# Performance work log

Measured on AMD Instinct MI355X. Metric: run time of the kernel, lower is better.

The kernel has to match this reference:

```python
import jax, jax.numpy as jnp
import numpy as np

B, N, K = 4, 1024, 512
HEADS, DH = 8, 64
HID = 2048
KAPPA = 1.0      # kappa_beta
ALPHA = 1e-3     # ffn_alpha (prior weight)
LAM = 1.0        # ffn_lambda_belief
NITER = 2        # ffn_n_iterations
EPS = 1e-8


def _ln(x, g, b):
    m = jnp.mean(x, axis=-1, keepdims=True)
    v = jnp.var(x, axis=-1, keepdims=True)
    return (x - m) * jax.lax.rsqrt(v + 1e-5) * g + b


def _transport(x, phi, G):
    # truncated exp(phi . G) applied to x without materializing (B,N,K,K)
    def Ax(y):
        return jnp.einsum('bng,gkl,bnl->bnk', phi, G, y)
    a1 = Ax(x)
    return x + a1 + 0.5 * Ax(a1)


def setup_inputs() -> dict:
    key = jax.random.key(0)
    ks = jax.random.split(key, 16)
    mu_q = jax.random.normal(ks[0], (B, N, K), dtype=jnp.float32)
    sigma_q = jax.random.uniform(ks[1], (B, N, K), minval=0.5, maxval=1.5, dtype=jnp.float32)
    phi = 0.1 * jax.random.normal(ks[2], (B, N, 3), dtype=jnp.float32)
    A = jax.random.normal(ks[3], (3, K, K), dtype=jnp.float32)
    generators = 0.05 * (A - jnp.transpose(A, (0, 2, 1)))  # antisymmetric Lie generators
    mask = jnp.broadcast_to(jnp.tril(jnp.ones((N, N), dtype=bool)), (B, N, N))  # causal
    mu_prior = jax.random.normal(ks[4], (B, N, K), dtype=jnp.float32)
    s = 0.02
    Wq = s * jax.random.normal(ks[5], (K, K), dtype=jnp.float32)
    Wk = s * jax.random.normal(ks[6], (K, K), dtype=jnp.float32)
    Wv = s * jax.random.normal(ks[7], (K, K), dtype=jnp.float32)
    Wo = s * jax.random.normal(ks[8], (K, K), dtype=jnp.float32)
    g1 = jnp.ones((K,), jnp.float32); be1 = jnp.zeros((K,), jnp.float32)
    g2 = jnp.ones((K,), jnp.float32); be2 = jnp.zeros((K,), jnp.float32)
    W1 = s * jax.random.normal(ks[9], (K, HID), dtype=jnp.float32)
    bh1 = jnp.zeros((HID,), jnp.float32)
    W2 = s * jax.random.normal(ks[10], (HID, K), dtype=jnp.float32)
    bh2 = jnp.zeros((K,), jnp.float32)
    lr = jnp.array(0.1, jnp.float32)  # learnable VFE step size
    return {'mu_q': mu_q, 'sigma_q': sigma_q, 'phi': phi, 'generators': generators,
            'mask': mask, 'mu_prior': mu_prior, 'Wq': Wq, 'Wk': Wk, 'Wv': Wv, 'Wo': Wo,
            'g1': g1, 'be1': be1, 'g2': g2, 'be2': be2,
            'W1': W1, 'bh1': bh1, 'W2': W2, 'bh2': bh2, 'lr': lr}


def reference(mu_q, sigma_q, phi, generators, mask, mu_prior,
              Wq, Wk, Wv, Wo, g1, be1, g2, be2, W1, bh1, W2, bh2, lr):
    # ---- attention sublayer ----
    mu_n = _ln(mu_q, g1, be1)
    mu_g = _transport(mu_n, phi, generators)  # transport to common frame

    def heads(x):  # (B,N,K) -> (B,H,N,Dh)
        return x.reshape(B, N, HEADS, DH).transpose(0, 2, 1, 3)

    q = heads(mu_g @ Wq)
    k = heads(mu_g @ Wk)
    v = heads(mu_g @ Wv)
    # diagonal covariance propagated through linear maps: var_out = sigma @ W^2
    sq = heads(sigma_q @ (Wq * Wq)) + EPS
    sk = heads(sigma_q @ (Wk * Wk)) + EPS

    inv = 1.0 / sq
    # KL(N(k_j,sk_j) || N(q_i,sq_i)) for diagonal Gaussians, decomposed into matmuls
    tr = jnp.einsum('bhid,bhjd->bhij', inv, sk)
    quad = (jnp.sum(q * q * inv, axis=-1)[..., None]
            - 2.0 * jnp.einsum('bhid,bhjd->bhij', q * inv, k)
            + jnp.einsum('bhid,bhjd->bhij', inv, k * k))
    logdet = (jnp.sum(jnp.log(sq), axis=-1)[..., None]
              - jnp.sum(jnp.log(sk), axis=-1)[:, :, None, :])
    kl = 0.5 * (tr + quad - DH + logdet)  # (B,H,N,N)

    scores = jnp.where(mask[:, None, :, :], -kl / KAPPA, -1e9)
    beta = jax.nn.softmax(scores, axis=-1)

    out = jnp.einsum('bhij,bhjd->bhid', beta, v)
    out = out.transpose(0, 2, 1, 3).reshape(B, N, K)
    mu_attn = _transport(out @ Wo, -phi, generators)  # back-transport to local frames
    mu_res = mu_q + mu_attn  # residual (dropout is identity in eval)

    # ---- VFE_dynamic FFN sublayer ----
    mu_n2 = _ln(mu_res, g2, be2)
    beta_m = jnp.mean(beta, axis=1)  # (B,N,N) attention-belief coupling
    h = mu_n2
    for _ in range(NITER):
        drive = jax.nn.gelu(h @ W1 + bh1) @ W2 + bh2
        grad = ALPHA * (h - mu_prior) + LAM * (h - jnp.einsum('bij,bjk->bik', beta_m, h))
        h = h + lr * (drive - grad)
    mu_out = mu_res + (h - mu_n2)

    return (mu_out, sigma_q, phi)
```

## Files before the change

### kernel.cpp

```cpp
#include <hip/hip_runtime.h>
#include <math.h>

#define BB 4
#define NN 1024
#define KK 512
#define HH 8
#define DHh 64
#define HIDd 2048
#define BN (BB*NN)

typedef unsigned short u16;
typedef __attribute__((ext_vector_type(8))) short bf16x8;
typedef __attribute__((ext_vector_type(4))) float f32x4;

__device__ __forceinline__ float gelu_tanh(float x){
    float x3 = x*x*x;
    float t = tanhf(0.7978845608028654f*(x + 0.044715f*x3));
    return 0.5f*x*(1.0f+t);
}
__device__ __forceinline__ u16 f2bf(float x){
    unsigned int u = __float_as_uint(x);
    unsigned int r = (u + 0x7fffu + ((u>>16)&1u)) >> 16;
    return (u16)r;
}
__device__ __forceinline__ float bf2f(u16 b){
    return __uint_as_float(((unsigned int)b)<<16);
}
__device__ __forceinline__ void gload16(const void* g, void* l){
    __builtin_amdgcn_global_load_lds((__attribute__((address_space(1))) void*)g,
                                     (__attribute__((address_space(3))) void*)l, 16, 0, 0);
}
__device__ __forceinline__ void wsplit(u16* hi, u16* lo, size_t o, float v){
    u16 h = f2bf(v);
    hi[o] = h;
    if (lo) lo[o] = f2bf(v - bf2f(h));
}

__global__ __launch_bounds__(256) void split_t_k(
    const float* __restrict__ src, u16* __restrict__ hi, u16* __restrict__ lo,
    int Kc, int Nc, long sS, long sD, int square)
{
    __shared__ float t[32][33];
    const int n0 = blockIdx.x*32, k0 = blockIdx.y*32, bz = blockIdx.z;
    const float* S = src + (long)bz*sS;
    const int tx = threadIdx.x & 31, ty = threadIdx.x >> 5;
    for (int r = ty; r < 32; r += 8){
        float v = S[(long)(k0+r)*Nc + n0+tx];
        if (square) v *= v;
        t[r][tx] = v;
    }
    __syncthreads();
    for (int r = ty; r < 32; r += 8){
        float v = t[tx][r];
        long o = (long)bz*sD + (long)(n0+r)*Kc + k0 + tx;
        wsplit(hi, lo, o, v);
    }
}

__global__ __launch_bounds__(256) void wmega_k(
    const float* __restrict__ Wq, const float* __restrict__ Wk,
    const float* __restrict__ Wv, const float* __restrict__ Wo,
    const float* __restrict__ W1, const float* __restrict__ W2,
    const float* __restrict__ gen,
    u16* __restrict__ WQKVh, u16* __restrict__ WQKVl, u16* __restrict__ WoTh,
    u16* __restrict__ WSQKh, u16* __restrict__ WSQKl,
    u16* __restrict__ W1Th, u16* __restrict__ W2Th, u16* __restrict__ GFh)
{
    const int z = blockIdx.z;
    const int tid = threadIdx.x;
    if (z == 8){
        if (blockIdx.x >= 48) return;
        const int c0 = blockIdx.x*32, k0 = blockIdx.y*32;
        const int tx = tid&31, ty = tid>>5;
        const int g = c0/KK, l0 = c0%KK;
        for (int r=ty; r<32; r+=8)
            GFh[(size_t)(k0+r)*(3*KK) + c0+tx] =
                f2bf(gen[(size_t)g*KK*KK + (size_t)(k0+r)*KK + l0+tx]);
        return;
    }
    __shared__ float t[32][33];
    const float* src; u16* hi; u16* lo=0; int sq=0;
    int n0, k0, Kc, Nc;
    const size_t KK2 = (size_t)KK*KK;
    if (z < 6){
        if (blockIdx.x >= 16) return;
        n0 = blockIdx.x*32; k0 = blockIdx.y*32; Kc=KK; Nc=KK;
        if      (z==0){ src=Wq; hi=WQKVh;       lo=WQKVl; }
        else if (z==1){ src=Wk; hi=WQKVh+KK2;   lo=WQKVl+KK2; }
        else if (z==2){ src=Wv; hi=WQKVh+2*KK2; lo=WQKVl+2*KK2; }
        else if (z==3){ src=Wo; hi=WoTh; }
        else if (z==4){ src=Wq; hi=WSQKh;       lo=WSQKl; sq=1; }
        else          { src=Wk; hi=WSQKh+KK2;   lo=WSQKl+KK2; sq=1; }
    } else if (z == 6){
        src=W1; hi=W1Th; Kc=KK; Nc=HIDd;
        n0 = blockIdx.x*32; k0 = blockIdx.y*32;
    } else {
        src=W2; hi=W2Th; Kc=HIDd; Nc=KK;
        n0 = blockIdx.y*32; k0 = blockIdx.x*32;
    }
    const int tx=tid&31, ty=tid>>5;
    for (int r=ty;r<32;r+=8){
        float v = src[(long)(k0+r)*Nc + n0+tx];
        if (sq) v*=v;
        t[r][tx]=v;
    }
    __syncthreads();
    for (int r=ty;r<32;r+=8){
        float v = t[tx][r];
        long o = (long)(n0+r)*Kc + k0+tx;
        wsplit(hi, lo, o, v);
    }
}

template<int PRODS>
__global__ __launch_bounds__(256) void gemm_mfma_k(
    const u16* __restrict__ Ah, const u16* __restrict__ Al,
    const u16* __restrict__ Bh, const u16* __restrict__ Bl,
    float* __restrict__ C, u16* __restrict__ Chi, u16* __restrict__ Clo,
    int M, int Kc, int Nc, int lda,
    long sA, long sB, long sC, const float* __restrict__ bias, int act,
    int cskip)
{
    __shared__ u16 shAh[2][128*32], shBh[2][128*32];
    constexpr int SLO = (PRODS==3) ? 2*128*32 : 8;
    __shared__ u16 shAl[SLO], shBl[SLO];
    const int m0 = blockIdx.x*128, n0 = blockIdx.y*128;
    if (cskip == 1 && n0 > m0 + 127) return;
    const int bz = blockIdx.z;
    const u16* gAh = Ah + (long)bz*sA;
    const u16* gBh = Bh + (long)bz*sB;
    const u16* gAl = (PRODS==3) ? Al + (long)bz*sA : nullptr;
    const u16* gBl = (PRODS==3) ? Bl + (long)bz*sB : nullptr;
    const int tid = threadIdx.x;
    const int wave = tid >> 6, lane = tid & 63;
    const int quad = lane >> 4, r16 = lane & 15;
    const int wm = (wave>>1)*64, wn = (wave&1)*64;

    f32x4 acc[4][4];
    #pragma unroll
    for (int i=0;i<4;i++)
        #pragma unroll
        for (int j=0;j<4;j++) acc[i][j] = (f32x4){0.f,0.f,0.f,0.f};

    auto stage = [&](int sel, int k0){
        #pragma unroll
        for (int half=0; half<2; ++half){
            int c = half*256 + tid;
            int row = c >> 2;
            int kg = ((c & 3) ^ ((row >> 1) & 3))*8;
            long ga = (long)(m0+row)*lda + k0 + kg;
            long gb = (long)(n0+row)*Kc + k0 + kg;
            gload16(gAh+ga, &shAh[sel][c*8]);
            gload16(gBh+gb, &shBh[sel][c*8]);
            if constexpr (PRODS==3){
                gload16(gAl+ga, &shAl[sel*128*32 + c*8]);
                gload16(gBl+gb, &shBl[sel*128*32 + c*8]);
            }
        }
    };

    const int nsteps = Kc >> 5;
    stage(0, 0);
    __syncthreads();
    int cur = 0;
    const int swz = (quad ^ ((r16 >> 1) & 3))*8;
    for (int t = 0; t < nsteps; ++t){
        if (t+1 < nsteps) stage(cur^1, (t+1)<<5);
        bf16x8 afh[4], bfh[4];
        #pragma unroll
        for (int i=0;i<4;i++){
            afh[i] = *(const bf16x8*)&shAh[cur][(wm+i*16+r16)*32 + swz];
            bfh[i] = *(const bf16x8*)&shBh[cur][(wn+i*16+r16)*32 + swz];
        }
        if constexpr (PRODS==3){
            bf16x8 afl[4], bfl[4];
            #pragma unroll
            for (int i=0;i<4;i++){
                afl[i] = *(const bf16x8*)&shAl[cur*128*32 + (wm+i*16+r16)*32 + swz];
                bfl[i] = *(const bf16x8*)&shBl[cur*128*32 + (wn+i*16+r16)*32 + swz];
            }
            #pragma unroll
            for (int i=0;i<4;i++)
                #pragma unroll
                for (int j=0;j<4;j++){
                    acc[i][j] = __builtin_amdgcn_mfma_f32_16x16x32_bf16(afh[i], bfh[j], acc[i][j], 0,0,0);
                    acc[i][j] = __builtin_amdgcn_mfma_f32_16x16x32_bf16(afh[i], bfl[j], acc[i][j], 0,0,0);
                    acc[i][j] = __builtin_amdgcn_mfma_f32_16x16x32_bf16(afl[i], bfh[j], acc[i][j], 0,0,0);
                }
        } else {
            #pragma unroll
            for (int i=0;i<4;i++)
                #pragma unroll
                for (int j=0;j<4;j++)
                    acc[i][j] = __builtin_amdgcn_mfma_f32_16x16x32_bf16(afh[i], bfh[j], acc[i][j], 0,0,0);
        }
        __syncthreads();
        cur ^= 1;
    }
    #pragma unroll
    for (int i=0;i<4;i++){
        #pragma unroll
        for (int j=0;j<4;j++){
            int gc = n0 + wn + j*16 + r16;
            if (gc >= Nc) continue;
            float bv = bias ? bias[gc] : 0.f;
            #pragma unroll
            for (int r=0;r<4;r++){
                long gr = m0 + wm + i*16 + quad*4 + r;
                float v = acc[i][j][r] + bv;
                if (act) v = gelu_tanh(v);
                long o = (long)bz*sC + gr*Nc + gc;
                if (C) C[o] = v;
                if (Chi){ u16 t = f2bf(v); Chi[o] = t; if (Clo) Clo[o] = f2bf(v - bf2f(t)); }
            }
        }
    }
}

__global__ __launch_bounds__(256) void gemm64_k(
    const u16* __restrict__ Ah, const u16* __restrict__ Bh,
    float* __restrict__ C, u16* __restrict__ Chi, u16* __restrict__ Clo,
    int M, int Kc, int Nc, int lda,
    long sA, long sB, long sC, const float* __restrict__ bias, int act,
    int ktrim,
    const float* __restrict__ phi, u16* __restrict__ X3e, float esign,
    const float* __restrict__ t_x, const float* __restrict__ t_a1,
    const float* __restrict__ t_res,
    const float* __restrict__ f_hin, const float* __restrict__ f_bmh,
    const float* __restrict__ f_mup, const float* __restrict__ f_lr,
    u16* __restrict__ f_hh, float* __restrict__ f_hout,
    const float* __restrict__ f_mrb, const float* __restrict__ f_mn2,
    float* __restrict__ f_out, int fmode)
{
    __shared__ u16 shA[2][64*64], shB[2][64*64];
    const int m0 = blockIdx.x*64, n0 = blockIdx.y*64;
    const int bz = blockIdx.z;
    const u16* gA = Ah + (long)bz*sA;
    const u16* gB = Bh + (long)bz*sB;
    const int tid = threadIdx.x;
    const int wave = tid >> 6, lane = tid & 63;
    const int quad = lane >> 4, r16 = lane & 15;
    const int wr = wave*16;
    const int kend = ktrim ? min(Kc, m0 + 64) : Kc;
    const int nsteps = kend >> 6;

    f32x4 acc[4];
    #pragma unroll
    for (int j=0;j<4;j++) acc[j] = (f32x4){0.f,0.f,0.f,0.f};

    auto stage = [&](int sel, int k0){
        #pragma unroll
        for (int rep=0; rep<2; ++rep){
            int c = rep*256 + tid;
            int row = c >> 3;
            int kg = ((c & 7) ^ (row & 7))*8;
            gload16(gA + (long)(m0+row)*lda + k0 + kg, &shA[sel][c*8]);
            gload16(gB + (long)(n0+row)*Kc + k0 + kg, &shB[sel][c*8]);
        }
    };

    stage(0, 0);
    __syncthreads();
    int cur = 0;
    for (int t = 0; t < nsteps; ++t){
        if (t+1 < nsteps) stage(cur^1, (t+1)<<6);
        #pragma unroll
        for (int kk=0; kk<2; ++kk){
            const int s = (((kk<<2)+quad) ^ (r16 & 7))*8;
            bf16x8 af = *(const bf16x8*)&shA[cur][(wr+r16)*64 + s];
            #pragma unroll
            for (int j=0;j<4;j++){
                bf16x8 bh = *(const bf16x8*)&shB[cur][(j*16+r16)*64 + s];
                acc[j] = __builtin_amdgcn_mfma_f32_16x16x32_bf16(af, bh, acc[j], 0,0,0);
            }
        }
        __syncthreads();
        cur ^= 1;
    }
    float lrv = 0.f;
    if (fmode) lrv = *f_lr;
    #pragma unroll
    for (int j=0;j<4;j++){
        int gc = n0 + j*16 + r16;
        float bv = bias ? bias[gc] : 0.f;
        #pragma unroll
        for (int r=0;r<4;r++){
            long gr = m0 + wr + quad*4 + r;
            float v = acc[j][r] + bv;
            if (act) v = gelu_tanh(v);
            long o = (long)bz*sC + gr*Nc + gc;
            if (t_x){
                v = t_x[o] + t_a1[o] + 0.5f*v;
                if (t_res) v += t_res[o];
            }
            if (fmode){
                float hv = f_hin[o];
                float val = hv + lrv*(v - (1e-3f*(hv - f_mup[o]) + (hv - f_bmh[o])));
                if (fmode == 1){ f_hout[o] = val; f_hh[o] = f2bf(val); }
                else           { f_out[o] = f_mrb[o] + val - f_mn2[o]; }
            } else {
                if (C) C[o] = v;
                if (Chi){ u16 t = f2bf(v); Chi[o] = t; if (Clo) Clo[o] = f2bf(v - bf2f(t)); }
                if (X3e){
                    const float* ph = phi + gr*3;
                    size_t b = (size_t)gr*(3*KK) + gc;
                    X3e[b]      = f2bf(esign*ph[0]*v);
                    X3e[b+KK]   = f2bf(esign*ph[1]*v);
                    X3e[b+2*KK] = f2bf(esign*ph[2]*v);
                }
            }
        }
    }
}

__global__ __launch_bounds__(256) void ln_k(
    const float* __restrict__ x, const float* __restrict__ g,
    const float* __restrict__ be, float* __restrict__ y,
    const float* __restrict__ phi, u16* __restrict__ x3, float esign,
    const float* __restrict__ sg, u16* __restrict__ sgh, u16* __restrict__ sgl,
    u16* __restrict__ yh16, float* __restrict__ osig, float* __restrict__ ophi)
{
    __shared__ float sh[8];
    const int r = blockIdx.x, tid = threadIdx.x;
    const float* xr = x + (long)r*KK;
    float2 v = *(const float2*)(xr + tid*2);
    float s = v.x+v.y, s2 = v.x*v.x+v.y*v.y;
    #pragma unroll
    for (int o=32;o>0;o>>=1){ s += __shfl_down(s,o); s2 += __shfl_down(s2,o); }
    if ((tid&63)==0){ sh[tid>>6]=s; sh[4+(tid>>6)]=s2; }
    __syncthreads();
    s  = sh[0]+sh[1]+sh[2]+sh[3];
    s2 = sh[4]+sh[5]+sh[6]+sh[7];
    const float mean = s*(1.f/KK);
    const float var  = s2*(1.f/KK) - mean*mean;
    const float rs = rsqrtf(var + 1e-5f);
    float2 gg = *(const float2*)(g + tid*2);
    float2 bb = *(const float2*)(be + tid*2);
    float ox = (v.x-mean)*rs*gg.x + bb.x;
    float oy = (v.y-mean)*rs*gg.y + bb.y;
    long o = (long)r*KK + tid*2;
    *(float2*)(y + o) = make_float2(ox, oy);
    if (yh16){ yh16[o] = f2bf(ox); yh16[o+1] = f2bf(oy); }
    if (x3){
        const float* ph = phi + r*3;
        size_t b = (size_t)r*(3*KK) + tid*2;
        #pragma unroll
        for (int gg2=0; gg2<3; ++gg2){
            float p = esign*ph[gg2];
            x3[b + gg2*KK]     = f2bf(p*ox);
            x3[b + gg2*KK + 1] = f2bf(p*oy);
        }
        if (ophi && tid < 3) ophi[(size_t)r*3 + tid] = phi[(size_t)r*3 + tid];
    }
    if (sgh){
        float2 sv = *(const float2*)(sg + o);
        wsplit(sgh, sgl, o,   sv.x);
        wsplit(sgh, sgl, o+1, sv.y);
        if (osig) *(float2*)(osig + o) = sv;
    }
}

__global__ __launch_bounds__(512) void prepvt_k(
    const float* __restrict__ QKV, const float* __restrict__ SQSK,
    u16* __restrict__ CFh, u16* __restrict__ CFl,
    u16* __restrict__ KSh, u16* __restrict__ KSl, float* __restrict__ dvec,
    u16* __restrict__ VTh)
{
    __shared__ float t[64][65];
    const int bx = blockIdx.x;
    const int tid = threadIdx.x;
    if (bx < BN){
        const int bn = bx;
        const int b = bn / NN, n = bn % NN;
        const int h = tid >> 6, d = tid & 63;
        float q  = QKV[(size_t)bn*1536 + h*DHh + d];
        float k  = QKV[(size_t)bn*1536 + KK + h*DHh + d];
        float sq = SQSK[(size_t)bn*1024 + h*DHh + d] + 1e-8f;
        float sk = SQSK[(size_t)bn*1024 + KK + h*DHh + d] + 1e-8f;
        float inv = 1.f/sq;
        float nqi = -2.f*q*inv;
        float skk = sk + k*k;
        const size_t base = ((size_t)(h*BB + b)*NN + n)*128;
        wsplit(CFh, CFl, base+d,    inv);
        wsplit(CFh, CFl, base+64+d, nqi);
        wsplit(KSh, KSl, base+d,    skk);
        wsplit(KSh, KSl, base+64+d, k);
        float dv = __logf(sk);
        #pragma unroll
        for (int o=32;o>0;o>>=1) dv += __shfl_down(dv,o);
        if (d==0) dvec[((size_t)h*BB + b)*NN + n] = dv;
        return;
    }
    const int idx = bx - BN;
    const int n0 = (idx & 15)*64;
    const int h = (idx>>4)&7;
    const int b = idx>>7;
    const int c4 = (tid & 15) * 4;
    const int r0 = tid >> 4;
    for (int rr = r0; rr < 64; rr += 32){
        float4 v = *(const float4*)(QKV + (size_t)(b*NN + n0 + rr)*1536 + 1024 + h*DHh + c4);
        t[c4+0][rr] = v.x; t[c4+1][rr] = v.y; t[c4+2][rr] = v.z; t[c4+3][rr] = v.w;
    }
    __syncthreads();
    for (int dd = r0; dd < 64; dd += 32){
        size_t base = ((size_t)(h*BB + b)*64 + dd)*NN + n0 + c4;
        #pragma unroll
        for (int q=0;q<4;q++) VTh[base+q] = f2bf(t[dd][c4+q]);
    }
}

__global__ __launch_bounds__(256) void softmax_all_k(
    float* __restrict__ S, const float* __restrict__ dvec, u16* __restrict__ BMh)
{
    __shared__ float s_sc[NN];
    __shared__ float s_bm[NN];
    __shared__ float s_red[4];
    const int tid = threadIdx.x;
    const int b = blockIdx.x / NN, i = blockIdx.x % NN;
    const int L = i + 1;
    const int JEND = ((i >> 6) + 1) << 6;
    for (int j=tid;j<JEND;j+=256) s_bm[j]=0.f;
    for (int h=0; h<8; ++h){
        const int z = h*BB + b;
        float* row = S + ((long)z*NN + i)*NN;
        const float* dp = dvec + (size_t)z*NN;
        float lm = -3.0e38f;
        for (int j=tid;j<L;j+=256){
            float sc = -0.5f*row[j] + 0.5f*dp[j];
            s_sc[j] = sc;
            lm = fmaxf(lm, sc);
        }
        #pragma unroll
        for (int o=32;o>0;o>>=1) lm = fmaxf(lm, __shfl_xor(lm, o));
        __syncthreads();
        if ((tid&63)==0) s_red[tid>>6] = lm;
        __syncthreads();
        const float mx = fmaxf(fmaxf(s_red[0],s_red[1]), fmaxf(s_red[2],s_red[3]));
        float ps = 0.f;
        for (int j=tid;j<L;j+=256){
            float e = __expf(s_sc[j]-mx);
            s_sc[j] = e;
            ps += e;
        }
        #pragma unroll
        for (int o=32;o>0;o>>=1) ps += __shfl_xor(ps, o);
        __syncthreads();
        if ((tid&63)==0) s_red[tid>>6] = ps;
        __syncthreads();
        const float isum = 1.f/(s_red[0]+s_red[1]+s_red[2]+s_red[3]);
        u16* brow = (u16*)row;
        for (int j=tid;j<JEND;j+=256){
            if (j < L){
                float w = s_sc[j]*isum;
                brow[j] = f2bf(w);
                s_bm[j] += 0.125f*w;
            } else {
                brow[j] = 0;
            }
        }
        __syncthreads();
    }
    const long bmrow = ((long)b*NN + i)*NN;
    for (int j=tid;j<JEND;j+=256) BMh[bmrow+j] = f2bf(s_bm[j]);
}

__global__ __launch_bounds__(256) void pv_k(
    const u16* __restrict__ Sbeta,
    const u16* __restrict__ VTh,
    u16* __restrict__ xh)
{
    __shared__ u16 shA[2][64*64], shB[2][64*64];
    const int m0 = blockIdx.x*64;
    const int z = blockIdx.y;
    const int b = z & 3, head = z >> 2;
    const int tid = threadIdx.x;
    const int wave = tid>>6, lane = tid&63;
    const int quad = lane>>4, r16 = lane&15;
    f32x4 acc[4];
    #pragma unroll
    for (int j=0;j<4;j++) acc[j]=(f32x4){0.f,0.f,0.f,0.f};
    const int nsteps = (m0 >> 6) + 1;

    auto stage = [&](int sel, int j0){
        #pragma unroll
        for (int rep=0; rep<2; ++rep){
            int c = rep*256 + tid;
            int row = c >> 3;
            int k8 = ((c & 7) ^ (row & 7))*8;
            gload16(Sbeta + ((size_t)(z*NN + m0 + row))*(2*NN) + j0 + k8, &shA[sel][c*8]);
            gload16(VTh + ((size_t)(z*64 + row))*NN + j0 + k8, &shB[sel][c*8]);
        }
    };

    stage(0, 0);
    __syncthreads();
    int cur = 0;
    for (int t = 0; t < nsteps; ++t){
        if (t+1 < nsteps) stage(cur^1, (t+1)<<6);
        #pragma unroll
        for (int kk=0; kk<2; ++kk){
            const int s = (((kk<<2)+quad) ^ (r16 & 7))*8;
            bf16x8 af = *(const bf16x8*)&shA[cur][(wave*16 + r16)*64 + s];
            #pragma unroll
            for (int nj=0; nj<4; ++nj){
                bf16x8 bh = *(const bf16x8*)&shB[cur][(nj*16 + r16)*64 + s];
                acc[nj] = __builtin_amdgcn_mfma_f32_16x16x32_bf16(af, bh, acc[nj], 0,0,0);
            }
        }
        __syncthreads();
        cur ^= 1;
    }
    #pragma unroll
    for (int nj=0;nj<4;nj++){
        #pragma unroll
        for (int r=0;r<4;r++){
            int i = m0 + wave*16 + quad*4 + r;
            int d = nj*16 + r16;
            size_t o = ((size_t)(b*NN)+i)*KK + head*64 + d;
            xh[o] = f2bf(acc[nj][r]);
        }
    }
}

extern "C" void kernel_launch(void* const* d_in, const int* in_sizes, int n_in,
                              void* d_out, int out_size, void* d_ws, size_t ws_size,
                              hipStream_t stream) {
    const float* mu_q    = (const float*)d_in[0];
    const float* sigma_q = (const float*)d_in[1];
    const float* phi     = (const float*)d_in[2];
    const float* gen     = (const float*)d_in[3];
    const float* mu_prior= (const float*)d_in[5];
    const float* Wq = (const float*)d_in[6];
    const float* Wk = (const float*)d_in[7];
    const float* Wv = (const float*)d_in[8];
    const float* Wo = (const float*)d_in[9];
    const float* g1 = (const float*)d_in[10];
    const float* be1= (const float*)d_in[11];
    const float* g2 = (const float*)d_in[12];
    const float* be2= (const float*)d_in[13];
    const float* W1 = (const float*)d_in[14];
    const float* bh1= (const float*)d_in[15];
    const float* W2 = (const float*)d_in[16];
    const float* bh2= (const float*)d_in[17];
    const float* lr = (const float*)d_in[18];
    float* out = (float*)d_out;

    float* w = (float*)d_ws;
    size_t off = 0;
    auto alloc = [&](size_t n){ float* p = w + off; off += (n+3)&~(size_t)3; return p; };
    auto ualloc = [&](size_t n){ return (u16*)alloc((n+1)/2); };

    float* Xb   = alloc((size_t)BN*KK);
    float* A1b  = alloc((size_t)BN*KK);
    float* A2b  = alloc((size_t)BN*KK);
    float* QKVb = alloc((size_t)BN*3*KK);
    float* SQSKb= alloc((size_t)BN*2*KK);
    float* REG  = alloc((size_t)16*NN*NN);
    float* Sbig = Xb;
    u16*  X3a   = (u16*)REG;
    u16*  X3b   = X3a + (size_t)BN*3*KK;
    u16*  SGh   = X3b + (size_t)BN*3*KK;
    u16*  SGl   = SGh + (size_t)BN*KK;
    u16*  ZH    = (u16*)REG;
    float* Db_  = alloc((size_t)HH*BB*NN);
    u16* AH  = ualloc((size_t)BN*HIDd); u16* AL  = ualloc((size_t)BN*HIDd);
    u16* CFh = AH;
    u16* CFl = AH + (size_t)HH*BB*NN*128;
    u16* KSh = AL;
    u16* KSl = AL + (size_t)HH*BB*NN*128;
    u16* VTh = ualloc((size_t)HH*BB*64*NN);
    u16* GFh = ualloc((size_t)3*KK*KK);
    u16* WQKVh= ualloc((size_t)3*KK*KK); u16* WQKVl= ualloc((size_t)3*KK*KK);
    u16* WSQKh= ualloc((size_t)2*KK*KK); u16* WSQKl= ualloc((size_t)2*KK*KK);
    u16* WoTh= ualloc((size_t)KK*KK);
    u16* W1Th= ualloc((size_t)KK*HIDd);
    u16* W2Th= ualloc((size_t)KK*HIDd);
    u16* BMh = ualloc((size_t)BB*NN*NN);
    u16* HTh = ualloc((size_t)BB*KK*NN);
    float* WOb = QKVb;
    float* Hb  = QKVb + (size_t)BN*KK;
    float* MRb = QKVb + 2*(size_t)BN*KK;
    float* MN2b= Xb;
    (void)A2b; (void)SQSKb;

    auto gemm64 = [&](const u16* ah, const u16* bh,
                      float* C, u16* chi, u16* clo, int M, int Kc, int Nc, int lda,
                      long sA, long sB, long sC, const float* bias, int act,
                      int ktrim, const float* xphi, u16* x3e, float esign,
                      const float* tx, const float* ta1, const float* tres, int batch){
        dim3 g(M/64, Nc/64, batch);
        gemm64_k<<<g, 256, 0, stream>>>(ah, bh, C, chi, clo,
                                        M, Kc, Nc, lda, sA, sB, sC, bias, act, ktrim,
                                        xphi, x3e, esign, tx, ta1, tres,
                                        0,0,0,0,0,0,0,0,0,0);
    };

    {
        dim3 gw(64, 16, 9);
        wmega_k<<<gw, 256, 0, stream>>>(Wq, Wk, Wv, Wo, W1, W2, gen,
                                        WQKVh, WQKVl, WoTh, WSQKh, WSQKl,
                                        W1Th, W2Th, GFh);
    }

    ln_k<<<BN, 256, 0, stream>>>(mu_q, g1, be1, Xb, phi, X3a, 1.f, sigma_q, SGh, SGl,
                                 0, out + (size_t)BN*KK, out + 2*(size_t)BN*KK);
    gemm64(X3a, GFh, A1b, 0,0, BN, 3*KK, KK, 3*KK, 0,0,0, nullptr, 0, 0,
           phi, X3b, 1.f, 0,0,0, 1);
    gemm64(X3b, GFh, 0, AH, AL, BN, 3*KK, KK, 3*KK, 0,0,0, nullptr, 0, 0,
           0, 0, 0.f, Xb, A1b, 0, 1);

    {
        dim3 gq(BN/128, (3*KK)/128, 1);
        gemm_mfma_k<3><<<gq, 256, 0, stream>>>(AH, AL, WQKVh, WQKVl, QKVb, 0, 0,
            BN, KK, 3*KK, KK, 0, 0, 0, nullptr, 0, 0);
        dim3 gs(BN/128, (2*KK)/128, 1);
        gemm_mfma_k<3><<<gs, 256, 0, stream>>>(SGh, SGl, WSQKh, WSQKl, SQSKb, 0, 0,
            BN, KK, 2*KK, KK, 0, 0, 0, nullptr, 0, 0);
    }
    prepvt_k<<<BN + 512, 512, 0, stream>>>(QKVb, SQSKb, CFh, CFl, KSh, KSl, Db_, VTh);

    {
        dim3 sg(NN/128, NN/128, 32);
        gemm_mfma_k<3><<<sg, 256, 0, stream>>>(CFh, CFl, KSh, KSl,
            Sbig, 0, 0, NN, 128, NN, 128,
            (long)NN*128, (long)NN*128, (long)NN*NN, nullptr, 0, 1);
        softmax_all_k<<<BB*NN, 256, 0, stream>>>(Sbig, Db_, BMh);
        dim3 pg(NN/64, 32, 1);
        pv_k<<<pg, 256, 0, stream>>>((const u16*)Sbig, VTh, AH);
    }

    gemm64(AH, WoTh, WOb, 0,0, BN, KK, KK, KK, 0,0,0, nullptr, 0, 0,
           phi, X3a, -1.f, 0,0,0, 1);
    gemm64(X3a, GFh, A1b, 0,0, BN, 3*KK, KK, 3*KK, 0,0,0, nullptr, 0, 0,
           phi, X3b, -1.f, 0,0,0, 1);
    gemm64(X3b, GFh, MRb, 0,0, BN, 3*KK, KK, 3*KK, 0,0,0, nullptr, 0, 0,
           0, 0, 0.f, WOb, A1b, mu_q, 1);
    ln_k<<<BN, 256, 0, stream>>>(MRb, g2, be2, MN2b, 0, 0, 0.f, 0, 0, 0,
                                 AH, 0, 0);

    for (int it=0; it<2; ++it){
        const float* hin = (it==0) ? MN2b : Hb;
        {
            dim3 tg(KK/32, NN/32, BB);
            split_t_k<<<tg, 256, 0, stream>>>(hin, HTh, 0, NN, KK,
                                              (long)NN*KK, (long)KK*NN, 0);
        }
        {
            dim3 bg(NN/64, KK/64, BB);
            gemm64_k<<<bg, 256, 0, stream>>>(BMh, HTh, A1b, 0,0,
                                             NN, NN, KK, NN,
                                             (long)NN*NN, (long)KK*NN, (long)NN*KK,
                                             nullptr, 0, 1, 0, 0, 0.f, 0,0,0,
                                             0,0,0,0,0,0,0,0,0,0);
        }
        {
            dim3 wg1(BN/128, HIDd/128, 1);
            gemm_mfma_k<1><<<wg1, 256, 0, stream>>>(AH, 0, W1Th, 0, 0, ZH, 0,
                BN, KK, HIDd, KK, 0, 0, 0, bh1, 1, 0);
        }
        {
            dim3 wg(BN/64, KK/64, 1);
            gemm64_k<<<wg, 256, 0, stream>>>(ZH, W2Th, 0,0,0,
                                             BN, HIDd, KK, HIDd, 0,0,0, bh2, 0, 0,
                                             0, 0, 0.f, 0,0,0,
                                             hin, A1b, mu_prior, lr, AH, Hb, MRb, MN2b, out,
                                             (it==0) ? 1 : 2);
        }
    }

    (void)in_sizes; (void)n_in; (void)out_size; (void)ws_size;
}
```

Baseline: 624.8 us.

## Fuse phi scaling into transport GEMM and serialize split-precision products over K

Adds a transport GEMM kernel that applies the per-row phi coefficients to the three generator segments inside the accumulation loop. This replaces the materialized 3K-wide phi-scaled input buffers (X3a/X3b) that were previously written and then re-read. The 3-product split-bf16 GEMM becomes a kernel that walks hi*hi, lo*hi and hi*lo as consecutive K segments through a single shared buffer pair, which halves LDS use and may raise occupancy. It also adds an x/y block-index flip on the FFN GEMMs so consecutive blocks walk along N, improving L2 reuse of the A rows, with some added indexing and loss of the hi-A fragment reuse.

```diff
diff --git a/kernel.cpp b/kernel.cpp
--- a/kernel.cpp
+++ b/kernel.cpp
@@ -112,25 +112,20 @@
     }
 }
 
-template<int PRODS>
 __global__ __launch_bounds__(256) void gemm_mfma_k(
-    const u16* __restrict__ Ah, const u16* __restrict__ Al,
-    const u16* __restrict__ Bh, const u16* __restrict__ Bl,
+    const u16* __restrict__ Ah, const u16* __restrict__ Bh,
     float* __restrict__ C, u16* __restrict__ Chi, u16* __restrict__ Clo,
     int M, int Kc, int Nc, int lda,
     long sA, long sB, long sC, const float* __restrict__ bias, int act,
-    int cskip)
-{
-    __shared__ u16 shAh[2][128*32], shBh[2][128*32];
-    constexpr int SLO = (PRODS==3) ? 2*128*32 : 8;
-    __shared__ u16 shAl[SLO], shBl[SLO];
-    const int m0 = blockIdx.x*128, n0 = blockIdx.y*128;
-    if (cskip == 1 && n0 > m0 + 127) return;
+    int xyflip)
+{
+    __shared__ u16 shA[2][128*32], shB[2][128*32];
+    const int bx = xyflip ? blockIdx.y : blockIdx.x;
+    const int by = xyflip ? blockIdx.x : blockIdx.y;
+    const int m0 = bx*128, n0 = by*128;
     const int bz = blockIdx.z;
     const u16* gAh = Ah + (long)bz*sA;
     const u16* gBh = Bh + (long)bz*sB;
-    const u16* gAl = (PRODS==3) ? Al + (long)bz*sA : nullptr;
-    const u16* gBl = (PRODS==3) ? Bl + (long)bz*sB : nullptr;
     const int tid = threadIdx.x;
     const int wave = tid >> 6, lane = tid & 63;
     const int quad = lane >> 4, r16 = lane & 15;
@@ -148,14 +143,8 @@
             int c = half*256 + tid;
             int row = c >> 2;
             int kg = ((c & 3) ^ ((row >> 1) & 3))*8;
-            long ga = (long)(m0+row)*lda + k0 + kg;
-            long gb = (long)(n0+row)*Kc + k0 + kg;
-            gload16(gAh+ga, &shAh[sel][c*8]);
-            gload16(gBh+gb, &shBh[sel][c*8]);
-            if constexpr (PRODS==3){
-                gload16(gAl+ga, &shAl[sel*128*32 + c*8]);
-                gload16(gBl+gb, &shBl[sel*128*32 + c*8]);
-            }
+            gload16(gAh + (long)(m0+row)*lda + k0 + kg, &shA[sel][c*8]);
+            gload16(gBh + (long)(n0+row)*Kc  + k0 + kg, &shB[sel][c*8]);
         }
     };
 
@@ -169,31 +158,14 @@
         bf16x8 afh[4], bfh[4];
         #pragma unroll
         for (int i=0;i<4;i++){
-            afh[i] = *(const bf16x8*)&shAh[cur][(wm+i*16+r16)*32 + swz];
-            bfh[i] = *(const bf16x8*)&shBh[cur][(wn+i*16+r16)*32 + swz];
-        }
-        if constexpr (PRODS==3){
-            bf16x8 afl[4], bfl[4];
+            afh[i] = *(const bf16x8*)&shA[cur][(wm+i*16+r16)*32 + swz];
+            bfh[i] = *(const bf16x8*)&shB[cur][(wn+i*16+r16)*32 + swz];
+        }
+        #pragma unroll
+        for (int i=0;i<4;i++)
             #pragma unroll
-            for (int i=0;i<4;i++){
-                afl[i] = *(const bf16x8*)&shAl[cur*128*32 + (wm+i*16+r16)*32 + swz];
-                bfl[i] = *(const bf16x8*)&shBl[cur*128*32 + (wn+i*16+r16)*32 + swz];
-            }
-            #pragma unroll
-            for (int i=0;i<4;i++)
-                #pragma unroll
-                for (int j=0;j<4;j++){
-                    acc[i][j] = __builtin_amdgcn_mfma_f32_16x16x32_bf16(afh[i], bfh[j], acc[i][j], 0,0,0);
-                    acc[i][j] = __builtin_amdgcn_mfma_f32_16x16x32_bf16(afh[i], bfl[j], acc[i][j], 0,0,0);
-                    acc[i][j] = __builtin_amdgcn_mfma_f32_16x16x32_bf16(afl[i], bfh[j], acc[i][j], 0,0,0);
-                }
-        } else {
-            #pragma unroll
-            for (int i=0;i<4;i++)
-                #pragma unroll
-                for (int j=0;j<4;j++)
-                    acc[i][j] = __builtin_amdgcn_mfma_f32_16x16x32_bf16(afh[i], bfh[j], acc[i][j], 0,0,0);
-        }
+            for (int j=0;j<4;j++)
+                acc[i][j] = __builtin_amdgcn_mfma_f32_16x16x32_bf16(afh[i], bfh[j], acc[i][j], 0,0,0);
         __syncthreads();
         cur ^= 1;
     }
@@ -217,15 +189,174 @@
     }
 }
 
+__global__ __launch_bounds__(256) void gemm_v3_k(
+    const u16* __restrict__ Ah, const u16* __restrict__ Al,
+    const u16* __restrict__ Bh, const u16* __restrict__ Bl,
+    float* __restrict__ C,
+    int M, int Kc, int Nc, int lda,
+    long sA, long sB, long sC, int cskip)
+{
+    __shared__ u16 shA[2][128*32], shB[2][128*32];
+    const int m0 = blockIdx.x*128, n0 = blockIdx.y*128;
+    if (cskip == 1 && n0 > m0 + 127) return;
+    const int bz = blockIdx.z;
+    const u16* gAh = Ah + (long)bz*sA;
+    const u16* gAl = Al + (long)bz*sA;
+    const u16* gBh = Bh + (long)bz*sB;
+    const u16* gBl = Bl + (long)bz*sB;
+    const int tid = threadIdx.x;
+    const int wave = tid >> 6, lane = tid & 63;
+    const int quad = lane >> 4, r16 = lane & 15;
+    const int wm = (wave>>1)*64, wn = (wave&1)*64;
+
+    f32x4 acc[4][4];
+    #pragma unroll
+    for (int i=0;i<4;i++)
+        #pragma unroll
+        for (int j=0;j<4;j++) acc[i][j] = (f32x4){0.f,0.f,0.f,0.f};
+
+    const int segsteps = Kc >> 5;
+    const int nsteps = 3*segsteps;
+    auto stage = [&](int sel, int t){
+        int seg = (t >= segsteps) + (t >= 2*segsteps);
+        int k0 = (t - seg*segsteps) << 5;
+        const u16* a = (seg==1) ? gAl : gAh;
+        const u16* b = (seg==2) ? gBl : gBh;
+        #pragma unroll
+        for (int half=0; half<2; ++half){
+            int c = half*256 + tid;
+            int row = c >> 2;
+            int kg = ((c & 3) ^ ((row >> 1) & 3))*8;
+            gload16(a + (long)(m0+row)*lda + k0 + kg, &shA[sel][c*8]);
+            gload16(b + (long)(n0+row)*Kc  + k0 + kg, &shB[sel][c*8]);
+        }
+    };
+
+    stage(0, 0);
+    __syncthreads();
+    int cur = 0;
+    const int swz = (quad ^ ((r16 >> 1) & 3))*8;
+    for (int t = 0; t < nsteps; ++t){
+        if (t+1 < nsteps) stage(cur^1, t+1);
+        bf16x8 afh[4], bfh[4];
+        #pragma unroll
+        for (int i=0;i<4;i++){
+            afh[i] = *(const bf16x8*)&shA[cur][(wm+i*16+r16)*32 + swz];
+            bfh[i] = *(const bf16x8*)&shB[cur][(wn+i*16+r16)*32 + swz];
+        }
+        #pragma unroll
+        for (int i=0;i<4;i++)
+            #pragma unroll
+            for (int j=0;j<4;j++)
+                acc[i][j] = __builtin_amdgcn_mfma_f32_16x16x32_bf16(afh[i], bfh[j], acc[i][j], 0,0,0);
+        __syncthreads();
+        cur ^= 1;
+    }
+    #pragma unroll
+    for (int i=0;i<4;i++){
+        #pragma unroll
+        for (int j=0;j<4;j++){
+            int gc = n0 + wn + j*16 + r16;
+            if (gc >= Nc) continue;
+            #pragma unroll
+            for (int r=0;r<4;r++){
+                long gr = m0 + wm + i*16 + quad*4 + r;
+                long o = (long)bz*sC + gr*Nc + gc;
+                C[o] = acc[i][j][r];
+            }
+        }
+    }
+}
+
+__global__ __launch_bounds__(256) void tgemm_k(
+    const u16* __restrict__ Ahh,
+    const u16* __restrict__ GFh,
+    const float* __restrict__ phi, float esign,
+    float* __restrict__ C, u16* __restrict__ Chi, u16* __restrict__ Clo,
+    const float* __restrict__ t_x, const float* __restrict__ t_a1,
+    const float* __restrict__ t_res)
+{
+    __shared__ u16 shA[2][64*64], shB[2][64*64];
+    const int m0 = blockIdx.x*64, n0 = blockIdx.y*64;
+    const int tid = threadIdx.x;
+    const int wave = tid >> 6, lane = tid & 63;
+    const int quad = lane >> 4, r16 = lane & 15;
+    const int wr = wave*16;
+
+    float ph[3][4];
+    #pragma unroll
+    for (int sgi=0; sgi<3; ++sgi)
+        #pragma unroll
+        for (int r=0; r<4; ++r)
+            ph[sgi][r] = esign*phi[(size_t)(m0+wr+quad*4+r)*3 + sgi];
+
+    f32x4 acc[4], tot[4];
+    #pragma unroll
+    for (int j=0;j<4;j++){ acc[j] = (f32x4){0.f,0.f,0.f,0.f}; tot[j] = acc[j]; }
+
+    auto stage = [&](int sel, int t){
+        int seg = t >> 3, k0 = (t & 7) << 6;
+        #pragma unroll
+        for (int rep=0; rep<2; ++rep){
+            int c = rep*256 + tid;
+            int row = c >> 3;
+            int kg = ((c & 7) ^ (row & 7))*8;
+            gload16(Ahh + (long)(m0+row)*KK + k0 + kg, &shA[sel][c*8]);
+            gload16(GFh + (long)(n0+row)*(3*KK) + seg*KK + k0 + kg, &shB[sel][c*8]);
+        }
+    };
+
+    stage(0, 0);
+    __syncthreads();
+    int cur = 0;
+    for (int t = 0; t < 24; ++t){
+        if (t+1 < 24) stage(cur^1, t+1);
+        #pragma unroll
+        for (int kk=0; kk<2; ++kk){
+            const int s = (((kk<<2)+quad) ^ (r16 & 7))*8;
+            bf16x8 af = *(const bf16x8*)&shA[cur][(wr+r16)*64 + s];
+            #pragma unroll
+            for (int j=0;j<4;j++){
+                bf16x8 bh = *(const bf16x8*)&shB[cur][(j*16+r16)*64 + s];
+                acc[j] = __builtin_amdgcn_mfma_f32_16x16x32_bf16(af, bh, acc[j], 0,0,0);
+            }
+        }
+        if ((t & 7) == 7){
+            int sgi = t >> 3;
+            #pragma unroll
+            for (int j=0;j<4;j++){
+                #pragma unroll
+                for (int r=0;r<4;r++) tot[j][r] += ph[sgi][r]*acc[j][r];
+                acc[j] = (f32x4){0.f,0.f,0.f,0.f};
+            }
+        }
+        __syncthreads();
+        cur ^= 1;
+    }
+    #pragma unroll
+    for (int j=0;j<4;j++){
+        int gc = n0 + j*16 + r16;
+        #pragma unroll
+        for (int r=0;r<4;r++){
+            long gr = m0 + wr + quad*4 + r;
+            float v = tot[j][r];
+            long o = gr*(long)KK + gc;
+            if (t_x){
+                v = t_x[o] + t_a1[o] + 0.5f*v;
+                if (t_res) v += t_res[o];
+            }
+            if (C) C[o] = v;
+            if (Chi){ u16 t2 = f2bf(v); Chi[o] = t2; if (Clo) Clo[o] = f2bf(v - bf2f(t2)); }
+        }
+    }
+}
+
 __global__ __launch_bounds__(256) void gemm64_k(
     const u16* __restrict__ Ah, const u16* __restrict__ Bh,
     float* __restrict__ C, u16* __restrict__ Chi, u16* __restrict__ Clo,
     int M, int Kc, int Nc, int lda,
     long sA, long sB, long sC, const float* __restrict__ bias, int act,
-    int ktrim,
-    const float* __restrict__ phi, u16* __restrict__ X3e, float esign,
-    const float* __restrict__ t_x, const float* __restrict__ t_a1,
-    const float* __restrict__ t_res,
+    int ktrim, int xyflip,
     const float* __restrict__ f_hin, const float* __restrict__ f_bmh,
     const float* __restrict__ f_mup, const float* __restrict__ f_lr,
     u16* __restrict__ f_hh, float* __restrict__ f_hout,
@@ -233,7 +364,9 @@
     float* __restrict__ f_out, int fmode)
 {
     __shared__ u16 shA[2][64*64], shB[2][64*64];
-    const int m0 = blockIdx.x*64, n0 = blockIdx.y*64;
+    const int bx = xyflip ? blockIdx.y : blockIdx.x;
+    const int by = xyflip ? blockIdx.x : blockIdx.y;
+    const int m0 = bx*64, n0 = by*64;
     const int bz = blockIdx.z;
     const u16* gA = Ah + (long)bz*sA;
     const u16* gB = Bh + (long)bz*sB;
@@ -289,10 +422,6 @@
             float v = acc[j][r] + bv;
             if (act) v = gelu_tanh(v);
             long o = (long)bz*sC + gr*Nc + gc;
-            if (t_x){
-                v = t_x[o] + t_a1[o] + 0.5f*v;
-                if (t_res) v += t_res[o];
-            }
             if (fmode){
                 float hv = f_hin[o];
                 float val = hv + lrv*(v - (1e-3f*(hv - f_mup[o]) + (hv - f_bmh[o])));
@@ -301,13 +430,6 @@
             } else {
                 if (C) C[o] = v;
                 if (Chi){ u16 t = f2bf(v); Chi[o] = t; if (Clo) Clo[o] = f2bf(v - bf2f(t)); }
-                if (X3e){
-                    const float* ph = phi + gr*3;
-                    size_t b = (size_t)gr*(3*KK) + gc;
-                    X3e[b]      = f2bf(esign*ph[0]*v);
-                    X3e[b+KK]   = f2bf(esign*ph[1]*v);
-                    X3e[b+2*KK] = f2bf(esign*ph[2]*v);
-                }
             }
         }
     }
@@ -316,9 +438,9 @@
 __global__ __launch_bounds__(256) void ln_k(
     const float* __restrict__ x, const float* __restrict__ g,
     const float* __restrict__ be, float* __restrict__ y,
-    const float* __restrict__ phi, u16* __restrict__ x3, float esign,
+    u16* __restrict__ yh16,
     const float* __restrict__ sg, u16* __restrict__ sgh, u16* __restrict__ sgl,
-    u16* __restrict__ yh16, float* __restrict__ osig, float* __restrict__ ophi)
+    float* __restrict__ osig, const float* __restrict__ phi, float* __restrict__ ophi)
 {
     __shared__ float sh[8];
     const int r = blockIdx.x, tid = threadIdx.x;
@@ -341,23 +463,13 @@
     long o = (long)r*KK + tid*2;
     *(float2*)(y + o) = make_float2(ox, oy);
     if (yh16){ yh16[o] = f2bf(ox); yh16[o+1] = f2bf(oy); }
-    if (x3){
-        const float* ph = phi + r*3;
-        size_t b = (size_t)r*(3*KK) + tid*2;
-        #pragma unroll
-        for (int gg2=0; gg2<3; ++gg2){
-            float p = esign*ph[gg2];
-            x3[b + gg2*KK]     = f2bf(p*ox);
-            x3[b + gg2*KK + 1] = f2bf(p*oy);
-        }
-        if (ophi && tid < 3) ophi[(size_t)r*3 + tid] = phi[(size_t)r*3 + tid];
-    }
     if (sgh){
         float2 sv = *(const float2*)(sg + o);
         wsplit(sgh, sgl, o,   sv.x);
         wsplit(sgh, sgl, o+1, sv.y);
         if (osig) *(float2*)(osig + o) = sv;
     }
+    if (ophi && tid < 3) ophi[(size_t)r*3 + tid] = phi[(size_t)r*3 + tid];
 }
 
 __global__ __launch_bounds__(512) void prepvt_k(
@@ -557,10 +669,11 @@
     float* SQSKb= alloc((size_t)BN*2*KK);
     float* REG  = alloc((size_t)16*NN*NN);
     float* Sbig = Xb;
-    u16*  X3a   = (u16*)REG;
-    u16*  X3b   = X3a + (size_t)BN*3*KK;
-    u16*  SGh   = X3b + (size_t)BN*3*KK;
+    u16*  SGh   = (u16*)REG;
     u16*  SGl   = SGh + (size_t)BN*KK;
+    u16*  Xh    = SGl + (size_t)BN*KK;
+    u16*  A1h   = Xh  + (size_t)BN*KK;
+    u16*  WOh   = A1h + (size_t)BN*KK;
     u16*  ZH    = (u16*)REG;
     float* Db_  = alloc((size_t)HH*BB*NN);
     u16* AH  = ualloc((size_t)BN*HIDd); u16* AL  = ualloc((size_t)BN*HIDd);
@@ -581,19 +694,7 @@
     float* Hb  = QKVb + (size_t)BN*KK;
     float* MRb = QKVb + 2*(size_t)BN*KK;
     float* MN2b= Xb;
-    (void)A2b; (void)SQSKb;
-
-    auto gemm64 = [&](const u16* ah, const u16* bh,
-                      float* C, u16* chi, u16* clo, int M, int Kc, int Nc, int lda,
-                      long sA, long sB, long sC, const float* bias, int act,
-                      int ktrim, const float* xphi, u16* x3e, float esign,
-                      const float* tx, const float* ta1, const float* tres, int batch){
-        dim3 g(M/64, Nc/64, batch);
-        gemm64_k<<<g, 256, 0, stream>>>(ah, bh, C, chi, clo,
-                                        M, Kc, Nc, lda, sA, sB, sC, bias, act, ktrim,
-                                        xphi, x3e, esign, tx, ta1, tres,
-                                        0,0,0,0,0,0,0,0,0,0);
-    };
+    (void)A2b;
 
     {
         dim3 gw(64, 16, 9);
@@ -602,41 +703,43 @@
                                         W1Th, W2Th, GFh);
     }
 
-    ln_k<<<BN, 256, 0, stream>>>(mu_q, g1, be1, Xb, phi, X3a, 1.f, sigma_q, SGh, SGl,
-                                 0, out + (size_t)BN*KK, out + 2*(size_t)BN*KK);
-    gemm64(X3a, GFh, A1b, 0,0, BN, 3*KK, KK, 3*KK, 0,0,0, nullptr, 0, 0,
-           phi, X3b, 1.f, 0,0,0, 1);
-    gemm64(X3b, GFh, 0, AH, AL, BN, 3*KK, KK, 3*KK, 0,0,0, nullptr, 0, 0,
-           0, 0, 0.f, Xb, A1b, 0, 1);
+    ln_k<<<BN, 256, 0, stream>>>(mu_q, g1, be1, Xb, Xh, sigma_q, SGh, SGl,
+                                 out + (size_t)BN*KK, phi, out + 2*(size_t)BN*KK);
+    {
+        dim3 tg(BN/64, KK/64, 1);
+        tgemm_k<<<tg, 256, 0, stream>>>(Xh, GFh, phi, 1.f, A1b, A1h, 0, 0, 0, 0);
+        tgemm_k<<<tg, 256, 0, stream>>>(A1h, GFh, phi, 1.f, 0, AH, AL, Xb, A1b, 0);
+    }
 
     {
         dim3 gq(BN/128, (3*KK)/128, 1);
-        gemm_mfma_k<3><<<gq, 256, 0, stream>>>(AH, AL, WQKVh, WQKVl, QKVb, 0, 0,
-            BN, KK, 3*KK, KK, 0, 0, 0, nullptr, 0, 0);
+        gemm_v3_k<<<gq, 256, 0, stream>>>(AH, AL, WQKVh, WQKVl, QKVb,
+            BN, KK, 3*KK, KK, 0, 0, 0, 0);
         dim3 gs(BN/128, (2*KK)/128, 1);
-        gemm_mfma_k<3><<<gs, 256, 0, stream>>>(SGh, SGl, WSQKh, WSQKl, SQSKb, 0, 0,
-            BN, KK, 2*KK, KK, 0, 0, 0, nullptr, 0, 0);
+        gemm_v3_k<<<gs, 256, 0, stream>>>(SGh, SGl, WSQKh, WSQKl, SQSKb,
+            BN, KK, 2*KK, KK, 0, 0, 0, 0);
     }
     prepvt_k<<<BN + 512, 512, 0, stream>>>(QKVb, SQSKb, CFh, CFl, KSh, KSl, Db_, VTh);
 
     {
         dim3 sg(NN/128, NN/128, 32);
-        gemm_mfma_k<3><<<sg, 256, 0, stream>>>(CFh, CFl, KSh, KSl,
-            Sbig, 0, 0, NN, 128, NN, 128,
-            (long)NN*128, (long)NN*128, (long)NN*NN, nullptr, 0, 1);
+        gemm_v3_k<<<sg, 256, 0, stream>>>(CFh, CFl, KSh, KSl, Sbig,
+            NN, 128, NN, 128, (long)NN*128, (long)NN*128, (long)NN*NN, 1);
         softmax_all_k<<<BB*NN, 256, 0, stream>>>(Sbig, Db_, BMh);
         dim3 pg(NN/64, 32, 1);
         pv_k<<<pg, 256, 0, stream>>>((const u16*)Sbig, VTh, AH);
     }
 
-    gemm64(AH, WoTh, WOb, 0,0, BN, KK, KK, KK, 0,0,0, nullptr, 0, 0,
-           phi, X3a, -1.f, 0,0,0, 1);
-    gemm64(X3a, GFh, A1b, 0,0, BN, 3*KK, KK, 3*KK, 0,0,0, nullptr, 0, 0,
-           phi, X3b, -1.f, 0,0,0, 1);
-    gemm64(X3b, GFh, MRb, 0,0, BN, 3*KK, KK, 3*KK, 0,0,0, nullptr, 0, 0,
-           0, 0, 0.f, WOb, A1b, mu_q, 1);
-    ln_k<<<BN, 256, 0, stream>>>(MRb, g2, be2, MN2b, 0, 0, 0.f, 0, 0, 0,
-                                 AH, 0, 0);
+    {
+        dim3 wg(BN/64, KK/64, 1);
+        gemm64_k<<<wg, 256, 0, stream>>>(AH, WoTh, WOb, WOh, 0,
+            BN, KK, KK, KK, 0,0,0, nullptr, 0, 0, 0,
+            0,0,0,0,0,0,0,0,0,0);
+        dim3 tg(BN/64, KK/64, 1);
+        tgemm_k<<<tg, 256, 0, stream>>>(WOh, GFh, phi, -1.f, A1b, A1h, 0, 0, 0, 0);
+        tgemm_k<<<tg, 256, 0, stream>>>(A1h, GFh, phi, -1.f, MRb, 0, 0, WOb, A1b, mu_q);
+    }
+    ln_k<<<BN, 256, 0, stream>>>(MRb, g2, be2, MN2b, AH, 0, 0, 0, 0, 0, 0);
 
     for (int it=0; it<2; ++it){
         const float* hin = (it==0) ? MN2b : Hb;
@@ -650,19 +753,18 @@
             gemm64_k<<<bg, 256, 0, stream>>>(BMh, HTh, A1b, 0,0,
                                              NN, NN, KK, NN,
                                              (long)NN*NN, (long)KK*NN, (long)NN*KK,
-                                             nullptr, 0, 1, 0, 0, 0.f, 0,0,0,
+                                             nullptr, 0, 1, 0,
                                              0,0,0,0,0,0,0,0,0,0);
         }
         {
-            dim3 wg1(BN/128, HIDd/128, 1);
-            gemm_mfma_k<1><<<wg1, 256, 0, stream>>>(AH, 0, W1Th, 0, 0, ZH, 0,
-                BN, KK, HIDd, KK, 0, 0, 0, bh1, 1, 0);
+            dim3 wg1(HIDd/128, BN/128, 1);
+            gemm_mfma_k<<<wg1, 256, 0, stream>>>(AH, W1Th, 0, ZH, 0,
+                BN, KK, HIDd, KK, 0, 0, 0, bh1, 1, 1);
         }
         {
-            dim3 wg(BN/64, KK/64, 1);
+            dim3 wg(KK/64, BN/64, 1);
             gemm64_k<<<wg, 256, 0, stream>>>(ZH, W2Th, 0,0,0,
-                                             BN, HIDd, KK, HIDd, 0,0,0, bh2, 0, 0,
-                                             0, 0, 0.f, 0,0,0,
+                                             BN, HIDd, KK, HIDd, 0,0,0, bh2, 0, 0, 1,
                                              hin, A1b, mu_prior, lr, AH, Hb, MRb, MN2b, out,
                                              (it==0) ? 1 : 2);
         }
```

Measured after the change: 639.3 us. 1.02x slower.
